# Kernel optimization log

Hardware: AMD Instinct MI355X
Metric: run time of the kernel (lower is better)

## Reference

```python
import jax, jax.numpy as jnp
import numpy as np

N = 20000   # nodes
E = 320000  # edges (before self-loops)
F_IN = 128  # in_feats
H = 4       # heads
C = 64      # hidden (per-head channels; concat=False averages heads)
G = 64      # graphs in batch
EPS = 1e-5  # BatchNorm eps


def _gat(x, src, dst, W, a_src, a_dst, bias):
    # PyG GATConv, concat=False: project, per-edge LeakyReLU attention,
    # segment-softmax over destination nodes, scatter-add, mean over heads.
    h = (x @ W).reshape(N, H, C)                    # [N,H,C]
    es = (h * a_src).sum(-1)                        # [N,H]
    ed = (h * a_dst).sum(-1)                        # [N,H]
    e = jax.nn.leaky_relu(es[src] + ed[dst], 0.2)   # [Etot,H]
    m = jax.ops.segment_max(e, dst, num_segments=N)
    m = jnp.where(jnp.isfinite(m), m, 0.0)          # nodes with no in-edges
    p = jnp.exp(e - m[dst])
    s = jax.ops.segment_sum(p, dst, num_segments=N)
    alpha = p / (s[dst] + 1e-16)                    # PyG softmax epsilon
    out = jax.ops.segment_sum(h[src] * alpha[:, :, None], dst, num_segments=N)
    return out.mean(axis=1) + bias                  # [N,C]


def _bn(x, g, b):
    # BatchNorm1d in training mode: biased batch statistics over nodes
    mu = x.mean(axis=0)
    var = ((x - mu) ** 2).mean(axis=0)
    return (x - mu) * jax.lax.rsqrt(var + EPS) * g + b


def setup_inputs() -> dict:
    key = jax.random.key(0)
    ks = jax.random.split(key, 16)
    x = jax.random.normal(ks[0], (N, F_IN), dtype=jnp.float32)
    edge_index = jax.random.randint(ks[1], (2, E), 0, N, dtype=jnp.int32)
    batch_idx = jnp.sort(jax.random.randint(ks[2], (N,), 0, G, dtype=jnp.int32))
    s1 = 1.0 / np.sqrt(F_IN)
    s2 = 1.0 / np.sqrt(C)
    return {
        "x": x,
        "W1": jax.random.normal(ks[3], (F_IN, H * C), jnp.float32) * s1,
        "a_src1": jax.random.normal(ks[4], (H, C), jnp.float32) * s2,
        "a_dst1": jax.random.normal(ks[5], (H, C), jnp.float32) * s2,
        "b1": jnp.zeros((C,), jnp.float32),
        "Wskip": jax.random.normal(ks[6], (F_IN, C), jnp.float32) * s1,
        "bskip": jnp.zeros((C,), jnp.float32),
        "g1": jnp.ones((C,), jnp.float32),
        "be1": jnp.zeros((C,), jnp.float32),
        "W2": jax.random.normal(ks[7], (C, H * C), jnp.float32) * s2,
        "a_src2": jax.random.normal(ks[8], (H, C), jnp.float32) * s2,
        "a_dst2": jax.random.normal(ks[9], (H, C), jnp.float32) * s2,
        "b2": jnp.zeros((C,), jnp.float32),
        "g2": jnp.ones((C,), jnp.float32),
        "be2": jnp.zeros((C,), jnp.float32),
        "edge_index": edge_index,
        "batch_idx": batch_idx,
    }


def reference(x, W1, a_src1, a_dst1, b1, Wskip, bskip, g1, be1,
              W2, a_src2, a_dst2, b2, g2, be2, edge_index, batch_idx):
    # add self-loops (PyG GATConv default add_self_loops=True)
    loop = jnp.arange(N, dtype=edge_index.dtype)
    src = jnp.concatenate([edge_index[0], loop])
    dst = jnp.concatenate([edge_index[1], loop])

    x0 = x
    h = _gat(x, src, dst, W1, a_src1, a_dst1, b1)
    h = jax.nn.gelu(_bn(h, g1, be1) + x0 @ Wskip + bskip, approximate=False)
    # dropout is identity in eval mode
    h2 = _gat(h, src, dst, W2, a_src2, a_dst2, b2)
    h2 = jax.nn.gelu(_bn(h2, g2, be2) + h, approximate=False)

    # global mean pool over graphs
    sums = jax.ops.segment_sum(h2, batch_idx, num_segments=G)
    cnts = jax.ops.segment_sum(jnp.ones((N,), h2.dtype), batch_idx, num_segments=G)
    return sums / jnp.maximum(cnts, 1.0)[:, None]
```

## Files before the change

kernel.cpp:

```cpp
#include <hip/hip_runtime.h>
#include <math.h>

#define NN   20000
#define EE   320000
#define ETOT 340000
#define FIN  128
#define HH   4
#define CC   64
#define HC   256
#define GG   64
#define BN_EPS 1e-5f
#define S1   384
#define S2   320
#define NBUCK 64
#define MAXDEG 64

typedef _Float16 v8h __attribute__((ext_vector_type(8)));
typedef _Float16 v4h __attribute__((ext_vector_type(4)));
typedef float    v4f __attribute__((ext_vector_type(4)));

__device__ __forceinline__ unsigned short f2bf(float f) {
    unsigned u = __float_as_uint(f);
    unsigned r = (u + 0x7FFF + ((u >> 16) & 1)) >> 16;
    return (unsigned short)r;
}
__device__ __forceinline__ float bf2f(unsigned short u) {
    return __uint_as_float((unsigned)u << 16);
}
__device__ __forceinline__ float gelu_exact(float v) {
    return 0.5f * v * (1.f + erff(v * 0.70710678118654752f));
}

__global__ __launch_bounds__(256) void pre1_kernel(
        const int* __restrict__ bidx, int* __restrict__ gstart,
        const float* __restrict__ W1, const float* __restrict__ Wskip,
        const float* __restrict__ W2,
        const float* __restrict__ as1, const float* __restrict__ ad1,
        const float* __restrict__ as2, const float* __restrict__ ad2,
        _Float16* __restrict__ BT1, _Float16* __restrict__ BT2,
        int* __restrict__ deg, float* __restrict__ sbuck1,
        float* __restrict__ sbuck2, float* __restrict__ outz) {
    int b = blockIdx.x, t = threadIdx.x;
    if (b < 79) {
        int i = b * 256 + t;
        if (i >= NN) return;
        int cur = bidx[i];
        if (i == 0) { for (int g = 0; g <= cur; ++g) gstart[g] = 0; }
        else { int prev = bidx[i - 1]; for (int g = prev + 1; g <= cur; ++g) gstart[g] = i; }
        if (i == NN - 1) { for (int g = cur + 1; g <= GG; ++g) gstart[g] = NN; }
    } else if (b < 271) {
        int i = (b - 79) * 256 + t;
        int col = i >> 7, k = i & 127;
        float v;
        if (col < 256) {
            v = W1[k * 256 + (col & 3) * 64 + (col >> 2)];
        } else if (col < 320) {
            v = Wskip[k * 64 + (col - 256)];
        } else if (col < 328) {
            int kk = col - 320, h = kk & 3;
            const float* av = (kk < 4 ? as1 : ad1) + h * 64;
            const float* wr = W1 + k * 256 + h * 64;
            float s = 0.f;
            #pragma unroll 8
            for (int c = 0; c < 64; ++c) s += wr[c] * av[c];
            v = s;
        } else v = 0.f;
        BT1[i] = (_Float16)v;
    } else if (b < 351) {
        int i = (b - 271) * 256 + t;
        int col = i >> 6, k = i & 63;
        float v;
        if (col < 256) {
            v = W2[k * 256 + (col & 3) * 64 + (col >> 2)];
        } else if (col < 264) {
            int kk = col - 256, h = kk & 3;
            const float* av = (kk < 4 ? as2 : ad2) + h * 64;
            const float* wr = W2 + k * 256 + h * 64;
            float s = 0.f;
            #pragma unroll 8
            for (int c = 0; c < 64; ++c) s += wr[c] * av[c];
            v = s;
        } else v = 0.f;
        BT2[i] = (_Float16)v;
    } else if (b < 367) {
        int i = (b - 351) * 256 + t;
        outz[i] = 0.f;
    } else if (b < 446) {
        int i = (b - 367) * 256 + t;
        if (i < NN) deg[i] = 0;
    } else if (b < 478) {
        int i = (b - 446) * 256 + t;
        sbuck1[i] = 0.f;
    } else {
        int i = (b - 478) * 256 + t;
        sbuck2[i] = 0.f;
    }
}

template<int NCB>
__global__ __launch_bounds__(256) void gemm_mfma(const float* __restrict__ A,
        const _Float16* __restrict__ BT, int M, int K,
        unsigned short* __restrict__ h4b, float* __restrict__ skipO,
        float* __restrict__ esf, float* __restrict__ edf,
        int escol0, int ngemm, int do_fill,
        const int* __restrict__ ei, int* __restrict__ deg,
        int* __restrict__ csr) {
    int b = blockIdx.x;
    int t = threadIdx.x;
    if (do_fill && b >= ngemm) {
        int i = (b - ngemm) * 256 + t;
        if (i >= ETOT) return;
        int s, d;
        if (i < EE) { s = ei[i]; d = ei[EE + i]; } else { s = i - EE; d = i - EE; }
        int p = atomicAdd(&deg[d], 1);
        if (p < MAXDEG) csr[d * MAXDEG + p] = s;
        return;
    }
    const int COLT = 2 * NCB * 16;
    __shared__ _Float16 sA[32][40];
    __shared__ _Float16 sBT[2 * NCB * 16][40];
    int tile = b & 1;
    int col0 = tile * COLT;
    int row0 = (b >> 1) * 32;
    int wave = t >> 6, lane = t & 63;
    int l15 = lane & 15, quad = lane >> 4;
    int rb  = wave & 1;
    int cb0 = (wave >> 1) * NCB;
    v4f acc[NCB] = {};
    for (int k0 = 0; k0 < K; k0 += 32) {
        {
            int r = t >> 3, c4 = t & 7;
            int gr = row0 + r;
            float4 v0 = make_float4(0.f, 0.f, 0.f, 0.f);
            if (gr < M) v0 = *(const float4*)&A[(size_t)gr * K + k0 + c4 * 4];
            v4h hv;
            hv[0] = (_Float16)v0.x; hv[1] = (_Float16)v0.y;
            hv[2] = (_Float16)v0.z; hv[3] = (_Float16)v0.w;
            *(v4h*)&sA[r][c4 * 4] = hv;
        }
        for (int j = t; j < COLT * 4; j += 256) {
            int c = j >> 2, s = j & 3;
            *(v8h*)&sBT[c][s * 8] = *(const v8h*)&BT[(size_t)(col0 + c) * K + k0 + s * 8];
        }
        __syncthreads();
        v8h af = *(const v8h*)&sA[rb * 16 + l15][quad * 8];
        #pragma unroll
        for (int c = 0; c < NCB; ++c) {
            v8h bf = *(const v8h*)&sBT[(cb0 + c) * 16 + l15][quad * 8];
            acc[c] = __builtin_amdgcn_mfma_f32_16x16x32_f16(af, bf, acc[c], 0, 0, 0);
        }
        __syncthreads();
    }
    #pragma unroll
    for (int c = 0; c < NCB; ++c) {
        int gcol = col0 + (cb0 + c) * 16 + l15;
        #pragma unroll
        for (int reg = 0; reg < 4; ++reg) {
            int gr = row0 + rb * 16 + quad * 4 + reg;
            if (gr >= M) continue;
            float v = acc[c][reg];
            if (gcol < 256) {
                h4b[(size_t)gr * HC + gcol] = f2bf(v);
            } else if (skipO != nullptr && gcol < 320) {
                skipO[(size_t)gr * CC + (gcol - 256)] = v;
            } else if (gcol >= escol0 && gcol < escol0 + 8) {
                if (gcol < escol0 + 4) esf[gr * 4 + (gcol - escol0)] = v;
                else                   edf[gr * 4 + (gcol - escol0 - 4)] = v;
            }
        }
    }
}

template<int NCB>
__global__ __launch_bounds__(256) void gemm_mfma_bn(const float* __restrict__ gout,
        const float* __restrict__ skip, const float* __restrict__ sbuck,
        const float* __restrict__ g, const float* __restrict__ be,
        const float* __restrict__ bskip, float* __restrict__ hmid,
        const _Float16* __restrict__ BT, int M, int K,
        unsigned short* __restrict__ h4b,
        float* __restrict__ esf, float* __restrict__ edf, int escol0) {
    const int COLT = 2 * NCB * 16;
    __shared__ _Float16 sA[32][40];
    __shared__ _Float16 sBT[2 * NCB * 16][40];
    __shared__ float tmp[128];
    __shared__ float sscale[64], sshift[64];
    int t = threadIdx.x;
    int b = blockIdx.x;
    if (t < 128) {
        float s = 0.f;
        #pragma unroll 16
        for (int k = 0; k < NBUCK; ++k) s += sbuck[k * 128 + t];
        tmp[t] = s;
    }
    __syncthreads();
    if (t < 64) {
        float mu  = tmp[t] * (1.f / NN);
        float var = tmp[64 + t] * (1.f / NN) - mu * mu;
        float inv = rsqrtf(var + BN_EPS) * g[t];
        sscale[t] = inv;
        sshift[t] = be[t] + bskip[t] - mu * inv;
    }
    __syncthreads();
    int tile = b & 1;
    int col0 = tile * COLT;
    int row0 = (b >> 1) * 32;
    int wave = t >> 6, lane = t & 63;
    int l15 = lane & 15, quad = lane >> 4;
    int rb  = wave & 1;
    int cb0 = (wave >> 1) * NCB;
    v4f acc[NCB] = {};
    for (int k0 = 0; k0 < K; k0 += 32) {
        {
            int r = t >> 3, c4 = t & 7;
            int gr = row0 + r;
            int cb = k0 + c4 * 4;
            float vv[4];
            if (gr < M) {
                float4 q = *(const float4*)&gout[(size_t)gr * CC + cb];
                float4 p = *(const float4*)&skip[(size_t)gr * CC + cb];
                float qa[4] = {q.x, q.y, q.z, q.w};
                float pa[4] = {p.x, p.y, p.z, p.w};
                #pragma unroll
                for (int u = 0; u < 4; ++u)
                    vv[u] = gelu_exact(qa[u] * sscale[cb + u] + sshift[cb + u] + pa[u]);
                if (tile == 0)
                    *(float4*)&hmid[(size_t)gr * CC + cb] =
                        make_float4(vv[0], vv[1], vv[2], vv[3]);
            } else {
                vv[0] = vv[1] = vv[2] = vv[3] = 0.f;
            }
            v4h hv;
            hv[0] = (_Float16)vv[0]; hv[1] = (_Float16)vv[1];
            hv[2] = (_Float16)vv[2]; hv[3] = (_Float16)vv[3];
            *(v4h*)&sA[r][c4 * 4] = hv;
        }
        for (int j = t; j < COLT * 4; j += 256) {
            int c = j >> 2, s = j & 3;
            *(v8h*)&sBT[c][s * 8] = *(const v8h*)&BT[(size_t)(col0 + c) * K + k0 + s * 8];
        }
        __syncthreads();
        v8h af = *(const v8h*)&sA[rb * 16 + l15][quad * 8];
        #pragma unroll
        for (int c = 0; c < NCB; ++c) {
            v8h bf = *(const v8h*)&sBT[(cb0 + c) * 16 + l15][quad * 8];
            acc[c] = __builtin_amdgcn_mfma_f32_16x16x32_f16(af, bf, acc[c], 0, 0, 0);
        }
        __syncthreads();
    }
    #pragma unroll
    for (int c = 0; c < NCB; ++c) {
        int gcol = col0 + (cb0 + c) * 16 + l15;
        #pragma unroll
        for (int reg = 0; reg < 4; ++reg) {
            int gr = row0 + rb * 16 + quad * 4 + reg;
            if (gr >= M) continue;
            float v = acc[c][reg];
            if (gcol < 256) {
                h4b[(size_t)gr * HC + gcol] = f2bf(v);
            } else if (gcol >= escol0 && gcol < escol0 + 8) {
                if (gcol < escol0 + 4) esf[gr * 4 + (gcol - escol0)] = v;
                else                   edf[gr * 4 + (gcol - escol0 - 4)] = v;
            }
        }
    }
}

__device__ __forceinline__ void edge_acc(const float4 esv, const ushort4 hv,
        const float4 edn, float4& acc, float4& ssum) {
    float e0 = esv.x + edn.x; e0 = fmaxf(e0, 0.2f * e0); float w0 = __expf(e0);
    float e1 = esv.y + edn.y; e1 = fmaxf(e1, 0.2f * e1); float w1 = __expf(e1);
    float e2 = esv.z + edn.z; e2 = fmaxf(e2, 0.2f * e2); float w2 = __expf(e2);
    float e3 = esv.w + edn.w; e3 = fmaxf(e3, 0.2f * e3); float w3 = __expf(e3);
    acc.x += w0 * bf2f(hv.x); ssum.x += w0;
    acc.y += w1 * bf2f(hv.y); ssum.y += w1;
    acc.z += w2 * bf2f(hv.z); ssum.z += w2;
    acc.w += w3 * bf2f(hv.w); ssum.w += w3;
}

__global__ __launch_bounds__(256) void aggr_kernel(const unsigned short* __restrict__ h4b,
        const float4* __restrict__ es4, const float4* __restrict__ ed4,
        const int* __restrict__ deg, const int* __restrict__ csr_src,
        const float* __restrict__ bias, float* __restrict__ out,
        float* __restrict__ sbuck) {
    int wave = threadIdx.x >> 6, lane = threadIdx.x & 63;
    int n = blockIdx.x * 4 + wave;
    float4 edn = ed4[n];
    float4 acc = make_float4(0.f, 0.f, 0.f, 0.f);
    float4 ssum = make_float4(0.f, 0.f, 0.f, 0.f);
    int dn = deg[n];
    dn = (dn < MAXDEG) ? dn : MAXDEG;
    int beg = n * MAXDEG, end = beg + dn;
    int j = beg;
    for (; j + 4 <= end; j += 4) {
        int s0 = csr_src[j + 0];
        int s1 = csr_src[j + 1];
        int s2 = csr_src[j + 2];
        int s3 = csr_src[j + 3];
        float4 E0 = es4[s0];
        float4 E1 = es4[s1];
        float4 E2 = es4[s2];
        float4 E3 = es4[s3];
        ushort4 v0 = *(const ushort4*)&h4b[(size_t)s0 * HC + lane * 4];
        ushort4 v1 = *(const ushort4*)&h4b[(size_t)s1 * HC + lane * 4];
        ushort4 v2 = *(const ushort4*)&h4b[(size_t)s2 * HC + lane * 4];
        ushort4 v3 = *(const ushort4*)&h4b[(size_t)s3 * HC + lane * 4];
        edge_acc(E0, v0, edn, acc, ssum);
        edge_acc(E1, v1, edn, acc, ssum);
        edge_acc(E2, v2, edn, acc, ssum);
        edge_acc(E3, v3, edn, acc, ssum);
    }
    for (; j < end; ++j) {
        int s = csr_src[j];
        float4 E = es4[s];
        ushort4 v = *(const ushort4*)&h4b[(size_t)s * HC + lane * 4];
        edge_acc(E, v, edn, acc, ssum);
    }
    float val = 0.25f * (acc.x / (ssum.x + 1e-16f) + acc.y / (ssum.y + 1e-16f) +
                         acc.z / (ssum.z + 1e-16f) + acc.w / (ssum.w + 1e-16f)) + bias[lane];
    out[n * CC + lane] = val;
    __shared__ float ls[4][64], lq[4][64];
    ls[wave][lane] = val;
    lq[wave][lane] = val * val;
    __syncthreads();
    if (wave == 0) {
        float s = ls[0][lane] + ls[1][lane] + ls[2][lane] + ls[3][lane];
        float q = lq[0][lane] + lq[1][lane] + lq[2][lane] + lq[3][lane];
        int bk = (blockIdx.x & (NBUCK - 1)) * 128;
        atomicAdd(&sbuck[bk + lane], s);
        atomicAdd(&sbuck[bk + 64 + lane], q);
    }
}

__global__ __launch_bounds__(256) void bnapply2_kernel(const float* __restrict__ gout,
        const float* __restrict__ sbuck, const float* __restrict__ g,
        const float* __restrict__ be, const float* __restrict__ resid,
        const int* __restrict__ bidx, const int* __restrict__ gstart,
        float* __restrict__ out) {
    __shared__ float tmp[128];
    __shared__ float smu[64], sinv[64];
    __shared__ float ls[4][64];
    __shared__ int gi[4];
    int t = threadIdx.x;
    if (t < 128) {
        float s = 0.f;
        #pragma unroll 16
        for (int k = 0; k < NBUCK; ++k) s += sbuck[k * 128 + t];
        tmp[t] = s;
    }
    __syncthreads();
    if (t < 64) {
        float mu  = tmp[t] * (1.f / NN);
        float var = tmp[64 + t] * (1.f / NN) - mu * mu;
        smu[t] = mu;
        sinv[t] = rsqrtf(var + BN_EPS) * g[t];
    }
    __syncthreads();
    int i = blockIdx.x * 256 + t;
    int ch = i & 63;
    int wave = t >> 6;
    int n = i >> 6;
    float v = (gout[i] - smu[ch]) * sinv[ch] + be[ch] + resid[i];
    v = gelu_exact(v);
    int gg = bidx[n];
    int cnt = gstart[gg + 1] - gstart[gg];
    ls[wave][ch] = v * (1.f / (float)cnt);
    if (ch == 0) gi[wave] = gg;
    __syncthreads();
    if (wave == 0) {
        if (gi[0] == gi[1] && gi[1] == gi[2] && gi[2] == gi[3]) {
            float s = ls[0][ch] + ls[1][ch] + ls[2][ch] + ls[3][ch];
            atomicAdd(&out[gi[0] * CC + ch], s);
        } else {
            #pragma unroll
            for (int w2 = 0; w2 < 4; ++w2)
                atomicAdd(&out[gi[w2] * CC + ch], ls[w2][ch]);
        }
    }
}

extern "C" void kernel_launch(void* const* d_in, const int* in_sizes, int n_in,
                              void* d_out, int out_size, void* d_ws, size_t ws_size,
                              hipStream_t stream) {
    const float* x      = (const float*)d_in[0];
    const float* W1     = (const float*)d_in[1];
    const float* a_src1 = (const float*)d_in[2];
    const float* a_dst1 = (const float*)d_in[3];
    const float* b1     = (const float*)d_in[4];
    const float* Wskip  = (const float*)d_in[5];
    const float* bskip  = (const float*)d_in[6];
    const float* g1     = (const float*)d_in[7];
    const float* be1    = (const float*)d_in[8];
    const float* W2     = (const float*)d_in[9];
    const float* a_src2 = (const float*)d_in[10];
    const float* a_dst2 = (const float*)d_in[11];
    const float* b2     = (const float*)d_in[12];
    const float* g2     = (const float*)d_in[13];
    const float* be2    = (const float*)d_in[14];
    const int*   ei     = (const int*)d_in[15];
    const int*   bidx   = (const int*)d_in[16];
    float* out = (float*)d_out;

    char* w = (char*)d_ws;
    size_t o = 0;
    auto alloc = [&](size_t bytes) -> void* {
        void* p = w + o;
        o = (o + bytes + 255) & ~(size_t)255;
        return p;
    };

    unsigned short* h4b = (unsigned short*)alloc((size_t)NN * HC * 2);
    float4* es4 = (float4*)alloc((size_t)NN * 16);
    float4* ed4 = (float4*)alloc((size_t)NN * 16);
    float* skip = (float*)alloc((size_t)NN * CC * 4);
    float* gout = (float*)alloc((size_t)NN * CC * 4);
    float* hmid = (float*)alloc((size_t)NN * CC * 4);
    _Float16* BT1 = (_Float16*)alloc((size_t)S1 * FIN * 2);
    _Float16* BT2 = (_Float16*)alloc((size_t)S2 * CC * 2);
    int* csr    = (int*)alloc((size_t)NN * MAXDEG * 4);
    int* gstart = (int*)alloc((size_t)(GG + 1) * 4);
    int* deg      = (int*)alloc((size_t)NN * 4);
    float* sbuck1 = (float*)alloc((size_t)NBUCK * 128 * 4);
    float* sbuck2 = (float*)alloc((size_t)NBUCK * 128 * 4);

    int ebk = (ETOT + 255) / 256;
    int nodeblk = NN / 4;

    pre1_kernel<<<510, 256, 0, stream>>>(bidx, gstart,
            W1, Wskip, W2, a_src1, a_dst1, a_src2, a_dst2, BT1, BT2,
            deg, sbuck1, sbuck2, out);

    gemm_mfma<6><<<1250 + ebk, 256, 0, stream>>>(x, BT1, NN, FIN,
            h4b, skip, (float*)es4, (float*)ed4, 320, 1250, 1, ei, deg, csr);
    aggr_kernel<<<nodeblk, 256, 0, stream>>>(h4b, es4, ed4, deg, csr, b1, gout,
            sbuck1);

    gemm_mfma_bn<5><<<1250, 256, 0, stream>>>(gout, skip, sbuck1, g1, be1, bskip,
            hmid, BT2, NN, CC, h4b, (float*)es4, (float*)ed4, 256);
    aggr_kernel<<<nodeblk, 256, 0, stream>>>(h4b, es4, ed4, deg, csr, b2, gout,
            sbuck2);
    bnapply2_kernel<<<NN * CC / 256, 256, 0, stream>>>(
        gout, sbuck2, g2, be2, hmid, bidx, gstart, out);
}
```

Measured before the change: 214.1 us.

## Fuse all stages into one persistent cooperative kernel with grid syncs

Replaces the six separate kernel launches (prep, GEMM1+CSR fill, aggregation, BN+GEMM2, aggregation, BN+pool) with a single cooperative persistent kernel that loops over work units and separates phases with grid.sync(). The aim is to remove per-launch overhead and inter-kernel gaps. In exchange, occupancy is capped by the cooperative grid size and by the register and shared-memory footprint of the merged kernel, and each grid-wide barrier has its own cost. The BN scale/shift is now computed once per block instead of once per GEMM block.

```diff
diff --git a/kernel.cpp b/kernel.cpp
--- a/kernel.cpp
+++ b/kernel.cpp
@@ -1,5 +1,8 @@
 #include <hip/hip_runtime.h>
+#include <hip/hip_cooperative_groups.h>
 #include <math.h>
+
+namespace cg = cooperative_groups;
 
 #define NN   20000
 #define EE   320000
@@ -14,6 +17,7 @@
 #define S2   320
 #define NBUCK 64
 #define MAXDEG 64
+#define EBK  1329
 
 typedef _Float16 v8h __attribute__((ext_vector_type(8)));
 typedef _Float16 v4h __attribute__((ext_vector_type(4)));
@@ -31,97 +35,34 @@
     return 0.5f * v * (1.f + erff(v * 0.70710678118654752f));
 }
 
-__global__ __launch_bounds__(256) void pre1_kernel(
-        const int* __restrict__ bidx, int* __restrict__ gstart,
-        const float* __restrict__ W1, const float* __restrict__ Wskip,
-        const float* __restrict__ W2,
-        const float* __restrict__ as1, const float* __restrict__ ad1,
-        const float* __restrict__ as2, const float* __restrict__ ad2,
-        _Float16* __restrict__ BT1, _Float16* __restrict__ BT2,
-        int* __restrict__ deg, float* __restrict__ sbuck1,
-        float* __restrict__ sbuck2, float* __restrict__ outz) {
-    int b = blockIdx.x, t = threadIdx.x;
-    if (b < 79) {
-        int i = b * 256 + t;
-        if (i >= NN) return;
-        int cur = bidx[i];
-        if (i == 0) { for (int g = 0; g <= cur; ++g) gstart[g] = 0; }
-        else { int prev = bidx[i - 1]; for (int g = prev + 1; g <= cur; ++g) gstart[g] = i; }
-        if (i == NN - 1) { for (int g = cur + 1; g <= GG; ++g) gstart[g] = NN; }
-    } else if (b < 271) {
-        int i = (b - 79) * 256 + t;
-        int col = i >> 7, k = i & 127;
-        float v;
-        if (col < 256) {
-            v = W1[k * 256 + (col & 3) * 64 + (col >> 2)];
-        } else if (col < 320) {
-            v = Wskip[k * 64 + (col - 256)];
-        } else if (col < 328) {
-            int kk = col - 320, h = kk & 3;
-            const float* av = (kk < 4 ? as1 : ad1) + h * 64;
-            const float* wr = W1 + k * 256 + h * 64;
-            float s = 0.f;
-            #pragma unroll 8
-            for (int c = 0; c < 64; ++c) s += wr[c] * av[c];
-            v = s;
-        } else v = 0.f;
-        BT1[i] = (_Float16)v;
-    } else if (b < 351) {
-        int i = (b - 271) * 256 + t;
-        int col = i >> 6, k = i & 63;
-        float v;
-        if (col < 256) {
-            v = W2[k * 256 + (col & 3) * 64 + (col >> 2)];
-        } else if (col < 264) {
-            int kk = col - 256, h = kk & 3;
-            const float* av = (kk < 4 ? as2 : ad2) + h * 64;
-            const float* wr = W2 + k * 256 + h * 64;
-            float s = 0.f;
-            #pragma unroll 8
-            for (int c = 0; c < 64; ++c) s += wr[c] * av[c];
-            v = s;
-        } else v = 0.f;
-        BT2[i] = (_Float16)v;
-    } else if (b < 367) {
-        int i = (b - 351) * 256 + t;
-        outz[i] = 0.f;
-    } else if (b < 446) {
-        int i = (b - 367) * 256 + t;
-        if (i < NN) deg[i] = 0;
-    } else if (b < 478) {
-        int i = (b - 446) * 256 + t;
-        sbuck1[i] = 0.f;
-    } else {
-        int i = (b - 478) * 256 + t;
-        sbuck2[i] = 0.f;
-    }
-}
-
-template<int NCB>
-__global__ __launch_bounds__(256) void gemm_mfma(const float* __restrict__ A,
+struct MegaParams {
+    const float* x;
+    const float* W1; const float* as1; const float* ad1; const float* b1;
+    const float* Wskip; const float* bskip; const float* g1; const float* be1;
+    const float* W2; const float* as2; const float* ad2; const float* b2;
+    const float* g2; const float* be2;
+    const int* ei; const int* bidx;
+    float* out;
+    unsigned short* h4b;
+    float4* es4; float4* ed4;
+    float* skip; float* gout; float* hmid;
+    _Float16* BT1; _Float16* BT2;
+    int* csr; int* gstart; int* deg;
+    float* sbuck1; float* sbuck2;
+};
+
+template<int NCB, bool BN>
+__device__ __forceinline__ void gemm_unit(int u,
+        const float* __restrict__ A, const float* __restrict__ skipIn,
+        float* __restrict__ hmid, const float* sscale, const float* sshift,
         const _Float16* __restrict__ BT, int M, int K,
         unsigned short* __restrict__ h4b, float* __restrict__ skipO,
-        float* __restrict__ esf, float* __restrict__ edf,
-        int escol0, int ngemm, int do_fill,
-        const int* __restrict__ ei, int* __restrict__ deg,
-        int* __restrict__ csr) {
-    int b = blockIdx.x;
-    int t = threadIdx.x;
-    if (do_fill && b >= ngemm) {
-        int i = (b - ngemm) * 256 + t;
-        if (i >= ETOT) return;
-        int s, d;
-        if (i < EE) { s = ei[i]; d = ei[EE + i]; } else { s = i - EE; d = i - EE; }
-        int p = atomicAdd(&deg[d], 1);
-        if (p < MAXDEG) csr[d * MAXDEG + p] = s;
-        return;
-    }
+        float* __restrict__ esf, float* __restrict__ edf, int escol0,
+        _Float16 (*sA)[40], _Float16 (*sBT)[40], int t) {
     const int COLT = 2 * NCB * 16;
-    __shared__ _Float16 sA[32][40];
-    __shared__ _Float16 sBT[2 * NCB * 16][40];
-    int tile = b & 1;
+    int tile = u & 1;
     int col0 = tile * COLT;
-    int row0 = (b >> 1) * 32;
+    int row0 = (u >> 1) * 32;
     int wave = t >> 6, lane = t & 63;
     int l15 = lane & 15, quad = lane >> 4;
     int rb  = wave & 1;
@@ -131,11 +72,28 @@
         {
             int r = t >> 3, c4 = t & 7;
             int gr = row0 + r;
-            float4 v0 = make_float4(0.f, 0.f, 0.f, 0.f);
-            if (gr < M) v0 = *(const float4*)&A[(size_t)gr * K + k0 + c4 * 4];
+            int cb = k0 + c4 * 4;
+            float vv[4] = {0.f, 0.f, 0.f, 0.f};
+            if (gr < M) {
+                if constexpr (BN) {
+                    float4 q = *(const float4*)&A[(size_t)gr * K + cb];
+                    float4 p = *(const float4*)&skipIn[(size_t)gr * K + cb];
+                    float qa[4] = {q.x, q.y, q.z, q.w};
+                    float pa[4] = {p.x, p.y, p.z, p.w};
+                    #pragma unroll
+                    for (int uu = 0; uu < 4; ++uu)
+                        vv[uu] = gelu_exact(qa[uu] * sscale[cb + uu] + sshift[cb + uu] + pa[uu]);
+                    if (tile == 0)
+                        *(float4*)&hmid[(size_t)gr * K + cb] =
+                            make_float4(vv[0], vv[1], vv[2], vv[3]);
+                } else {
+                    float4 v0 = *(const float4*)&A[(size_t)gr * K + cb];
+                    vv[0] = v0.x; vv[1] = v0.y; vv[2] = v0.z; vv[3] = v0.w;
+                }
+            }
             v4h hv;
-            hv[0] = (_Float16)v0.x; hv[1] = (_Float16)v0.y;
-            hv[2] = (_Float16)v0.z; hv[3] = (_Float16)v0.w;
+            hv[0] = (_Float16)vv[0]; hv[1] = (_Float16)vv[1];
+            hv[2] = (_Float16)vv[2]; hv[3] = (_Float16)vv[3];
             *(v4h*)&sA[r][c4 * 4] = hv;
         }
         for (int j = t; j < COLT * 4; j += 256) {
@@ -171,100 +129,6 @@
     }
 }
 
-template<int NCB>
-__global__ __launch_bounds__(256) void gemm_mfma_bn(const float* __restrict__ gout,
-        const float* __restrict__ skip, const float* __restrict__ sbuck,
-        const float* __restrict__ g, const float* __restrict__ be,
-        const float* __restrict__ bskip, float* __restrict__ hmid,
-        const _Float16* __restrict__ BT, int M, int K,
-        unsigned short* __restrict__ h4b,
-        float* __restrict__ esf, float* __restrict__ edf, int escol0) {
-    const int COLT = 2 * NCB * 16;
-    __shared__ _Float16 sA[32][40];
-    __shared__ _Float16 sBT[2 * NCB * 16][40];
-    __shared__ float tmp[128];
-    __shared__ float sscale[64], sshift[64];
-    int t = threadIdx.x;
-    int b = blockIdx.x;
-    if (t < 128) {
-        float s = 0.f;
-        #pragma unroll 16
-        for (int k = 0; k < NBUCK; ++k) s += sbuck[k * 128 + t];
-        tmp[t] = s;
-    }
-    __syncthreads();
-    if (t < 64) {
-        float mu  = tmp[t] * (1.f / NN);
-        float var = tmp[64 + t] * (1.f / NN) - mu * mu;
-        float inv = rsqrtf(var + BN_EPS) * g[t];
-        sscale[t] = inv;
-        sshift[t] = be[t] + bskip[t] - mu * inv;
-    }
-    __syncthreads();
-    int tile = b & 1;
-    int col0 = tile * COLT;
-    int row0 = (b >> 1) * 32;
-    int wave = t >> 6, lane = t & 63;
-    int l15 = lane & 15, quad = lane >> 4;
-    int rb  = wave & 1;
-    int cb0 = (wave >> 1) * NCB;
-    v4f acc[NCB] = {};
-    for (int k0 = 0; k0 < K; k0 += 32) {
-        {
-            int r = t >> 3, c4 = t & 7;
-            int gr = row0 + r;
-            int cb = k0 + c4 * 4;
-            float vv[4];
-            if (gr < M) {
-                float4 q = *(const float4*)&gout[(size_t)gr * CC + cb];
-                float4 p = *(const float4*)&skip[(size_t)gr * CC + cb];
-                float qa[4] = {q.x, q.y, q.z, q.w};
-                float pa[4] = {p.x, p.y, p.z, p.w};
-                #pragma unroll
-                for (int u = 0; u < 4; ++u)
-                    vv[u] = gelu_exact(qa[u] * sscale[cb + u] + sshift[cb + u] + pa[u]);
-                if (tile == 0)
-                    *(float4*)&hmid[(size_t)gr * CC + cb] =
-                        make_float4(vv[0], vv[1], vv[2], vv[3]);
-            } else {
-                vv[0] = vv[1] = vv[2] = vv[3] = 0.f;
-            }
-            v4h hv;
-            hv[0] = (_Float16)vv[0]; hv[1] = (_Float16)vv[1];
-            hv[2] = (_Float16)vv[2]; hv[3] = (_Float16)vv[3];
-            *(v4h*)&sA[r][c4 * 4] = hv;
-        }
-        for (int j = t; j < COLT * 4; j += 256) {
-            int c = j >> 2, s = j & 3;
-            *(v8h*)&sBT[c][s * 8] = *(const v8h*)&BT[(size_t)(col0 + c) * K + k0 + s * 8];
-        }
-        __syncthreads();
-        v8h af = *(const v8h*)&sA[rb * 16 + l15][quad * 8];
-        #pragma unroll
-        for (int c = 0; c < NCB; ++c) {
-            v8h bf = *(const v8h*)&sBT[(cb0 + c) * 16 + l15][quad * 8];
-            acc[c] = __builtin_amdgcn_mfma_f32_16x16x32_f16(af, bf, acc[c], 0, 0, 0);
-        }
-        __syncthreads();
-    }
-    #pragma unroll
-    for (int c = 0; c < NCB; ++c) {
-        int gcol = col0 + (cb0 + c) * 16 + l15;
-        #pragma unroll
-        for (int reg = 0; reg < 4; ++reg) {
-            int gr = row0 + rb * 16 + quad * 4 + reg;
-            if (gr >= M) continue;
-            float v = acc[c][reg];
-            if (gcol < 256) {
-                h4b[(size_t)gr * HC + gcol] = f2bf(v);
-            } else if (gcol >= escol0 && gcol < escol0 + 8) {
-                if (gcol < escol0 + 4) esf[gr * 4 + (gcol - escol0)] = v;
-                else                   edf[gr * 4 + (gcol - escol0 - 4)] = v;
-            }
-        }
-    }
-}
-
 __device__ __forceinline__ void edge_acc(const float4 esv, const ushort4 hv,
         const float4 edn, float4& acc, float4& ssum) {
     float e0 = esv.x + edn.x; e0 = fmaxf(e0, 0.2f * e0); float w0 = __expf(e0);
@@ -277,13 +141,13 @@
     acc.w += w3 * bf2f(hv.w); ssum.w += w3;
 }
 
-__global__ __launch_bounds__(256) void aggr_kernel(const unsigned short* __restrict__ h4b,
+__device__ __forceinline__ void aggr_unit(int u, const unsigned short* __restrict__ h4b,
         const float4* __restrict__ es4, const float4* __restrict__ ed4,
         const int* __restrict__ deg, const int* __restrict__ csr_src,
         const float* __restrict__ bias, float* __restrict__ out,
-        float* __restrict__ sbuck) {
-    int wave = threadIdx.x >> 6, lane = threadIdx.x & 63;
-    int n = blockIdx.x * 4 + wave;
+        float* __restrict__ sbuck, float* sls, int t) {
+    int wave = t >> 6, lane = t & 63;
+    int n = u * 4 + wave;
     float4 edn = ed4[n];
     float4 acc = make_float4(0.f, 0.f, 0.f, 0.f);
     float4 ssum = make_float4(0.f, 0.f, 0.f, 0.f);
@@ -318,62 +182,181 @@
     float val = 0.25f * (acc.x / (ssum.x + 1e-16f) + acc.y / (ssum.y + 1e-16f) +
                          acc.z / (ssum.z + 1e-16f) + acc.w / (ssum.w + 1e-16f)) + bias[lane];
     out[n * CC + lane] = val;
-    __shared__ float ls[4][64], lq[4][64];
+    float (*ls)[64] = (float (*)[64])sls;
+    float (*lq)[64] = (float (*)[64])(sls + 256);
     ls[wave][lane] = val;
     lq[wave][lane] = val * val;
     __syncthreads();
     if (wave == 0) {
         float s = ls[0][lane] + ls[1][lane] + ls[2][lane] + ls[3][lane];
         float q = lq[0][lane] + lq[1][lane] + lq[2][lane] + lq[3][lane];
-        int bk = (blockIdx.x & (NBUCK - 1)) * 128;
+        int bk = (u & (NBUCK - 1)) * 128;
         atomicAdd(&sbuck[bk + lane], s);
         atomicAdd(&sbuck[bk + 64 + lane], q);
     }
-}
-
-__global__ __launch_bounds__(256) void bnapply2_kernel(const float* __restrict__ gout,
-        const float* __restrict__ sbuck, const float* __restrict__ g,
-        const float* __restrict__ be, const float* __restrict__ resid,
-        const int* __restrict__ bidx, const int* __restrict__ gstart,
-        float* __restrict__ out) {
-    __shared__ float tmp[128];
-    __shared__ float smu[64], sinv[64];
-    __shared__ float ls[4][64];
+    __syncthreads();
+}
+
+__global__ __launch_bounds__(256) void mega(MegaParams P) {
+    cg::grid_group grid = cg::this_grid();
+    __shared__ __align__(16) unsigned char smem[17920];
+    __shared__ float sS[64], sH[64];
     __shared__ int gi[4];
     int t = threadIdx.x;
-    if (t < 128) {
-        float s = 0.f;
-        #pragma unroll 16
-        for (int k = 0; k < NBUCK; ++k) s += sbuck[k * 128 + t];
-        tmp[t] = s;
-    }
-    __syncthreads();
-    if (t < 64) {
-        float mu  = tmp[t] * (1.f / NN);
-        float var = tmp[64 + t] * (1.f / NN) - mu * mu;
-        smu[t] = mu;
-        sinv[t] = rsqrtf(var + BN_EPS) * g[t];
-    }
-    __syncthreads();
-    int i = blockIdx.x * 256 + t;
-    int ch = i & 63;
-    int wave = t >> 6;
-    int n = i >> 6;
-    float v = (gout[i] - smu[ch]) * sinv[ch] + be[ch] + resid[i];
-    v = gelu_exact(v);
-    int gg = bidx[n];
-    int cnt = gstart[gg + 1] - gstart[gg];
-    ls[wave][ch] = v * (1.f / (float)cnt);
-    if (ch == 0) gi[wave] = gg;
-    __syncthreads();
-    if (wave == 0) {
-        if (gi[0] == gi[1] && gi[1] == gi[2] && gi[2] == gi[3]) {
-            float s = ls[0][ch] + ls[1][ch] + ls[2][ch] + ls[3][ch];
-            atomicAdd(&out[gi[0] * CC + ch], s);
+    int nG = gridDim.x;
+
+    for (int u = blockIdx.x; u < 510; u += nG) {
+        if (u < 79) {
+            int i = u * 256 + t;
+            if (i < NN) {
+                int cur = P.bidx[i];
+                if (i == 0) { for (int g = 0; g <= cur; ++g) P.gstart[g] = 0; }
+                else { int prev = P.bidx[i - 1]; for (int g = prev + 1; g <= cur; ++g) P.gstart[g] = i; }
+                if (i == NN - 1) { for (int g = cur + 1; g <= GG; ++g) P.gstart[g] = NN; }
+            }
+        } else if (u < 271) {
+            int i = (u - 79) * 256 + t;
+            int col = i >> 7, k = i & 127;
+            float v;
+            if (col < 256) {
+                v = P.W1[k * 256 + (col & 3) * 64 + (col >> 2)];
+            } else if (col < 320) {
+                v = P.Wskip[k * 64 + (col - 256)];
+            } else if (col < 328) {
+                int kk = col - 320, h = kk & 3;
+                const float* av = (kk < 4 ? P.as1 : P.ad1) + h * 64;
+                const float* wr = P.W1 + k * 256 + h * 64;
+                float sdot = 0.f;
+                #pragma unroll 8
+                for (int c = 0; c < 64; ++c) sdot += wr[c] * av[c];
+                v = sdot;
+            } else v = 0.f;
+            P.BT1[i] = (_Float16)v;
+        } else if (u < 351) {
+            int i = (u - 271) * 256 + t;
+            int col = i >> 6, k = i & 63;
+            float v;
+            if (col < 256) {
+                v = P.W2[k * 256 + (col & 3) * 64 + (col >> 2)];
+            } else if (col < 264) {
+                int kk = col - 256, h = kk & 3;
+                const float* av = (kk < 4 ? P.as2 : P.ad2) + h * 64;
+                const float* wr = P.W2 + k * 256 + h * 64;
+                float sdot = 0.f;
+                #pragma unroll 8
+                for (int c = 0; c < 64; ++c) sdot += wr[c] * av[c];
+                v = sdot;
+            } else v = 0.f;
+            P.BT2[i] = (_Float16)v;
+        } else if (u < 367) {
+            int i = (u - 351) * 256 + t;
+            P.out[i] = 0.f;
+        } else if (u < 446) {
+            int i = (u - 367) * 256 + t;
+            if (i < NN) P.deg[i] = 0;
+        } else if (u < 478) {
+            int i = (u - 446) * 256 + t;
+            P.sbuck1[i] = 0.f;
         } else {
-            #pragma unroll
-            for (int w2 = 0; w2 < 4; ++w2)
-                atomicAdd(&out[gi[w2] * CC + ch], ls[w2][ch]);
+            int i = (u - 478) * 256 + t;
+            P.sbuck2[i] = 0.f;
+        }
+    }
+    grid.sync();
+
+    _Float16 (*sA)[40]  = (_Float16 (*)[40])smem;
+    _Float16 (*sBT)[40] = (_Float16 (*)[40])(smem + 32 * 40 * 2);
+    float* sls = (float*)smem;
+
+    for (int u = blockIdx.x; u < 1250 + EBK; u += nG) {
+        if (u < 1250) {
+            gemm_unit<6, false>(u, P.x, nullptr, nullptr, nullptr, nullptr,
+                P.BT1, NN, FIN, P.h4b, P.skip, (float*)P.es4, (float*)P.ed4, 320,
+                sA, sBT, t);
+        } else {
+            int i = (u - 1250) * 256 + t;
+            if (i < ETOT) {
+                int s, d;
+                if (i < EE) { s = P.ei[i]; d = P.ei[EE + i]; } else { s = i - EE; d = i - EE; }
+                int pp = atomicAdd(&P.deg[d], 1);
+                if (pp < MAXDEG) P.csr[d * MAXDEG + pp] = s;
+            }
+        }
+    }
+    grid.sync();
+
+    for (int u = blockIdx.x; u < 5000; u += nG)
+        aggr_unit(u, P.h4b, P.es4, P.ed4, P.deg, P.csr, P.b1, P.gout, P.sbuck1, sls, t);
+    grid.sync();
+
+    {
+        float* tmp = (float*)smem;
+        if (t < 128) {
+            float s = 0.f;
+            #pragma unroll 16
+            for (int k = 0; k < NBUCK; ++k) s += P.sbuck1[k * 128 + t];
+            tmp[t] = s;
+        }
+        __syncthreads();
+        if (t < 64) {
+            float mu  = tmp[t] * (1.f / NN);
+            float var = tmp[64 + t] * (1.f / NN) - mu * mu;
+            float inv = rsqrtf(var + BN_EPS) * P.g1[t];
+            sS[t] = inv;
+            sH[t] = P.be1[t] + P.bskip[t] - mu * inv;
+        }
+        __syncthreads();
+    }
+    for (int u = blockIdx.x; u < 1250; u += nG)
+        gemm_unit<5, true>(u, P.gout, P.skip, P.hmid, sS, sH,
+            P.BT2, NN, CC, P.h4b, nullptr, (float*)P.es4, (float*)P.ed4, 256,
+            sA, sBT, t);
+    grid.sync();
+
+    for (int u = blockIdx.x; u < 5000; u += nG)
+        aggr_unit(u, P.h4b, P.es4, P.ed4, P.deg, P.csr, P.b2, P.gout, P.sbuck2, sls, t);
+    grid.sync();
+
+    {
+        float* tmp = (float*)smem;
+        if (t < 128) {
+            float s = 0.f;
+            #pragma unroll 16
+            for (int k = 0; k < NBUCK; ++k) s += P.sbuck2[k * 128 + t];
+            tmp[t] = s;
+        }
+        __syncthreads();
+        if (t < 64) {
+            float mu  = tmp[t] * (1.f / NN);
+            float var = tmp[64 + t] * (1.f / NN) - mu * mu;
+            sS[t] = mu;
+            sH[t] = rsqrtf(var + BN_EPS) * P.g2[t];
+        }
+        __syncthreads();
+        float (*ls)[64] = (float (*)[64])smem;
+        for (int u = blockIdx.x; u < 5000; u += nG) {
+            int i = u * 256 + t;
+            int ch = i & 63;
+            int wave = t >> 6;
+            int n = i >> 6;
+            float v = (P.gout[i] - sS[ch]) * sH[ch] + P.be2[ch] + P.hmid[i];
+            v = gelu_exact(v);
+            int gg = P.bidx[n];
+            int cnt = P.gstart[gg + 1] - P.gstart[gg];
+            ls[wave][ch] = v * (1.f / (float)cnt);
+            if (ch == 0) gi[wave] = gg;
+            __syncthreads();
+            if (wave == 0) {
+                if (gi[0] == gi[1] && gi[1] == gi[2] && gi[2] == gi[3]) {
+                    float s4 = ls[0][ch] + ls[1][ch] + ls[2][ch] + ls[3][ch];
+                    atomicAdd(&P.out[gi[0] * CC + ch], s4);
+                } else {
+                    #pragma unroll
+                    for (int w2 = 0; w2 < 4; ++w2)
+                        atomicAdd(&P.out[gi[w2] * CC + ch], ls[w2][ch]);
+                }
+            }
+            __syncthreads();
         }
     }
 }
@@ -381,24 +364,25 @@
 extern "C" void kernel_launch(void* const* d_in, const int* in_sizes, int n_in,
                               void* d_out, int out_size, void* d_ws, size_t ws_size,
                               hipStream_t stream) {
-    const float* x      = (const float*)d_in[0];
-    const float* W1     = (const float*)d_in[1];
-    const float* a_src1 = (const float*)d_in[2];
-    const float* a_dst1 = (const float*)d_in[3];
-    const float* b1     = (const float*)d_in[4];
-    const float* Wskip  = (const float*)d_in[5];
-    const float* bskip  = (const float*)d_in[6];
-    const float* g1     = (const float*)d_in[7];
-    const float* be1    = (const float*)d_in[8];
-    const float* W2     = (const float*)d_in[9];
-    const float* a_src2 = (const float*)d_in[10];
-    const float* a_dst2 = (const float*)d_in[11];
-    const float* b2     = (const float*)d_in[12];
-    const float* g2     = (const float*)d_in[13];
-    const float* be2    = (const float*)d_in[14];
-    const int*   ei     = (const int*)d_in[15];
-    const int*   bidx   = (const int*)d_in[16];
-    float* out = (float*)d_out;
+    MegaParams P;
+    P.x      = (const float*)d_in[0];
+    P.W1     = (const float*)d_in[1];
+    P.as1    = (const float*)d_in[2];
+    P.ad1    = (const float*)d_in[3];
+    P.b1     = (const float*)d_in[4];
+    P.Wskip  = (const float*)d_in[5];
+    P.bskip  = (const float*)d_in[6];
+    P.g1     = (const float*)d_in[7];
+    P.be1    = (const float*)d_in[8];
+    P.W2     = (const float*)d_in[9];
+    P.as2    = (const float*)d_in[10];
+    P.ad2    = (const float*)d_in[11];
+    P.b2     = (const float*)d_in[12];
+    P.g2     = (const float*)d_in[13];
+    P.be2    = (const float*)d_in[14];
+    P.ei     = (const int*)d_in[15];
+    P.bidx   = (const int*)d_in[16];
+    P.out    = (float*)d_out;
 
     char* w = (char*)d_ws;
     size_t o = 0;
@@ -407,37 +391,32 @@
         o = (o + bytes + 255) & ~(size_t)255;
         return p;
     };
-
-    unsigned short* h4b = (unsigned short*)alloc((size_t)NN * HC * 2);
-    float4* es4 = (float4*)alloc((size_t)NN * 16);
-    float4* ed4 = (float4*)alloc((size_t)NN * 16);
-    float* skip = (float*)alloc((size_t)NN * CC * 4);
-    float* gout = (float*)alloc((size_t)NN * CC * 4);
-    float* hmid = (float*)alloc((size_t)NN * CC * 4);
-    _Float16* BT1 = (_Float16*)alloc((size_t)S1 * FIN * 2);
-    _Float16* BT2 = (_Float16*)alloc((size_t)S2 * CC * 2);
-    int* csr    = (int*)alloc((size_t)NN * MAXDEG * 4);
-    int* gstart = (int*)alloc((size_t)(GG + 1) * 4);
-    int* deg      = (int*)alloc((size_t)NN * 4);
-    float* sbuck1 = (float*)alloc((size_t)NBUCK * 128 * 4);
-    float* sbuck2 = (float*)alloc((size_t)NBUCK * 128 * 4);
-
-    int ebk = (ETOT + 255) / 256;
-    int nodeblk = NN / 4;
-
-    pre1_kernel<<<510, 256, 0, stream>>>(bidx, gstart,
-            W1, Wskip, W2, a_src1, a_dst1, a_src2, a_dst2, BT1, BT2,
-            deg, sbuck1, sbuck2, out);
-
-    gemm_mfma<6><<<1250 + ebk, 256, 0, stream>>>(x, BT1, NN, FIN,
-            h4b, skip, (float*)es4, (float*)ed4, 320, 1250, 1, ei, deg, csr);
-    aggr_kernel<<<nodeblk, 256, 0, stream>>>(h4b, es4, ed4, deg, csr, b1, gout,
-            sbuck1);
-
-    gemm_mfma_bn<5><<<1250, 256, 0, stream>>>(gout, skip, sbuck1, g1, be1, bskip,
-            hmid, BT2, NN, CC, h4b, (float*)es4, (float*)ed4, 256);
-    aggr_kernel<<<nodeblk, 256, 0, stream>>>(h4b, es4, ed4, deg, csr, b2, gout,
-            sbuck2);
-    bnapply2_kernel<<<NN * CC / 256, 256, 0, stream>>>(
-        gout, sbuck2, g2, be2, hmid, bidx, gstart, out);
-}
+    P.h4b  = (unsigned short*)alloc((size_t)NN * HC * 2);
+    P.es4  = (float4*)alloc((size_t)NN * 16);
+    P.ed4  = (float4*)alloc((size_t)NN * 16);
+    P.skip = (float*)alloc((size_t)NN * CC * 4);
+    P.gout = (float*)alloc((size_t)NN * CC * 4);
+    P.hmid = (float*)alloc((size_t)NN * CC * 4);
+    P.BT1  = (_Float16*)alloc((size_t)S1 * FIN * 2);
+    P.BT2  = (_Float16*)alloc((size_t)S2 * CC * 2);
+    P.csr  = (int*)alloc((size_t)NN * MAXDEG * 4);
+    P.gstart = (int*)alloc((size_t)(GG + 1) * 4);
+    P.deg    = (int*)alloc((size_t)NN * 4);
+    P.sbuck1 = (float*)alloc((size_t)NBUCK * 128 * 4);
+    P.sbuck2 = (float*)alloc((size_t)NBUCK * 128 * 4);
+
+    static int gblocks = 0;
+    if (gblocks == 0) {
+        int nb = 0, dev = 0, cus = 0;
+        hipGetDevice(&dev);
+        hipDeviceGetAttribute(&cus, hipDeviceAttributeMultiprocessorCount, dev);
+        hipOccupancyMaxActiveBlocksPerMultiprocessor(&nb, mega, 256, 0);
+        if (cus <= 0) cus = 256;
+        if (nb <= 0) nb = 1;
+        long long g = (long long)nb * cus;
+        if (g > 2048) g = 2048;
+        gblocks = (int)g;
+    }
+    void* args[] = { (void*)&P };
+    hipLaunchCooperativeKernel(mega, dim3(gblocks), dim3(256), args, 0, stream);
+}
```

Result: slower. 610.9 us (+185.3%).

## Store projected features head-major so each lane aggregates one head's channels

Applied to the files above, without the earlier changes.

The packed weight matrices now keep W1/W2 columns in natural head-major order instead of an interleaved channel-major order. The aggregation kernel changes to match: each lane handles four channels of a single head, so it loads one scalar attention logit per edge and computes one exp instead of four. The per-node results are then reduced across heads with cross-lane shuffles, and only 16 lanes write float4 outputs. This cuts redundant exp and softmax-sum work per edge, at the cost of shuffle reductions and fewer active lanes in the epilogue.

```diff
diff --git a/kernel.cpp b/kernel.cpp
--- a/kernel.cpp
+++ b/kernel.cpp
@@ -53,7 +53,7 @@
         int col = i >> 7, k = i & 127;
         float v;
         if (col < 256) {
-            v = W1[k * 256 + (col & 3) * 64 + (col >> 2)];
+            v = W1[k * 256 + col];
         } else if (col < 320) {
             v = Wskip[k * 64 + (col - 256)];
         } else if (col < 328) {
@@ -71,7 +71,7 @@
         int col = i >> 6, k = i & 63;
         float v;
         if (col < 256) {
-            v = W2[k * 256 + (col & 3) * 64 + (col >> 2)];
+            v = W2[k * 256 + col];
         } else if (col < 264) {
             int kk = col - 256, h = kk & 3;
             const float* av = (kk < 4 ? as2 : ad2) + h * 64;
@@ -265,28 +265,17 @@
     }
 }
 
-__device__ __forceinline__ void edge_acc(const float4 esv, const ushort4 hv,
-        const float4 edn, float4& acc, float4& ssum) {
-    float e0 = esv.x + edn.x; e0 = fmaxf(e0, 0.2f * e0); float w0 = __expf(e0);
-    float e1 = esv.y + edn.y; e1 = fmaxf(e1, 0.2f * e1); float w1 = __expf(e1);
-    float e2 = esv.z + edn.z; e2 = fmaxf(e2, 0.2f * e2); float w2 = __expf(e2);
-    float e3 = esv.w + edn.w; e3 = fmaxf(e3, 0.2f * e3); float w3 = __expf(e3);
-    acc.x += w0 * bf2f(hv.x); ssum.x += w0;
-    acc.y += w1 * bf2f(hv.y); ssum.y += w1;
-    acc.z += w2 * bf2f(hv.z); ssum.z += w2;
-    acc.w += w3 * bf2f(hv.w); ssum.w += w3;
-}
-
 __global__ __launch_bounds__(256) void aggr_kernel(const unsigned short* __restrict__ h4b,
-        const float4* __restrict__ es4, const float4* __restrict__ ed4,
+        const float* __restrict__ esf, const float* __restrict__ edf,
         const int* __restrict__ deg, const int* __restrict__ csr_src,
         const float* __restrict__ bias, float* __restrict__ out,
         float* __restrict__ sbuck) {
     int wave = threadIdx.x >> 6, lane = threadIdx.x & 63;
+    int head = lane >> 4;
     int n = blockIdx.x * 4 + wave;
-    float4 edn = ed4[n];
+    float edn = edf[n * 4 + head];
     float4 acc = make_float4(0.f, 0.f, 0.f, 0.f);
-    float4 ssum = make_float4(0.f, 0.f, 0.f, 0.f);
+    float ssum = 0.f;
     int dn = deg[n];
     dn = (dn < MAXDEG) ? dn : MAXDEG;
     int beg = n * MAXDEG, end = beg + dn;
@@ -296,31 +285,54 @@
         int s1 = csr_src[j + 1];
         int s2 = csr_src[j + 2];
         int s3 = csr_src[j + 3];
-        float4 E0 = es4[s0];
-        float4 E1 = es4[s1];
-        float4 E2 = es4[s2];
-        float4 E3 = es4[s3];
+        float E0 = esf[s0 * 4 + head];
+        float E1 = esf[s1 * 4 + head];
+        float E2 = esf[s2 * 4 + head];
+        float E3 = esf[s3 * 4 + head];
         ushort4 v0 = *(const ushort4*)&h4b[(size_t)s0 * HC + lane * 4];
         ushort4 v1 = *(const ushort4*)&h4b[(size_t)s1 * HC + lane * 4];
         ushort4 v2 = *(const ushort4*)&h4b[(size_t)s2 * HC + lane * 4];
         ushort4 v3 = *(const ushort4*)&h4b[(size_t)s3 * HC + lane * 4];
-        edge_acc(E0, v0, edn, acc, ssum);
-        edge_acc(E1, v1, edn, acc, ssum);
-        edge_acc(E2, v2, edn, acc, ssum);
-        edge_acc(E3, v3, edn, acc, ssum);
+        float e0 = E0 + edn; e0 = fmaxf(e0, 0.2f * e0); float w0 = __expf(e0);
+        float e1 = E1 + edn; e1 = fmaxf(e1, 0.2f * e1); float w1 = __expf(e1);
+        float e2 = E2 + edn; e2 = fmaxf(e2, 0.2f * e2); float w2 = __expf(e2);
+        float e3 = E3 + edn; e3 = fmaxf(e3, 0.2f * e3); float w3 = __expf(e3);
+        acc.x += w0 * bf2f(v0.x); acc.y += w0 * bf2f(v0.y);
+        acc.z += w0 * bf2f(v0.z); acc.w += w0 * bf2f(v0.w); ssum += w0;
+        acc.x += w1 * bf2f(v1.x); acc.y += w1 * bf2f(v1.y);
+        acc.z += w1 * bf2f(v1.z); acc.w += w1 * bf2f(v1.w); ssum += w1;
+        acc.x += w2 * bf2f(v2.x); acc.y += w2 * bf2f(v2.y);
+        acc.z += w2 * bf2f(v2.z); acc.w += w2 * bf2f(v2.w); ssum += w2;
+        acc.x += w3 * bf2f(v3.x); acc.y += w3 * bf2f(v3.y);
+        acc.z += w3 * bf2f(v3.z); acc.w += w3 * bf2f(v3.w); ssum += w3;
     }
     for (; j < end; ++j) {
         int s = csr_src[j];
-        float4 E = es4[s];
+        float E = esf[s * 4 + head];
         ushort4 v = *(const ushort4*)&h4b[(size_t)s * HC + lane * 4];
-        edge_acc(E, v, edn, acc, ssum);
-    }
-    float val = 0.25f * (acc.x / (ssum.x + 1e-16f) + acc.y / (ssum.y + 1e-16f) +
-                         acc.z / (ssum.z + 1e-16f) + acc.w / (ssum.w + 1e-16f)) + bias[lane];
-    out[n * CC + lane] = val;
+        float e = E + edn; e = fmaxf(e, 0.2f * e); float w = __expf(e);
+        acc.x += w * bf2f(v.x); acc.y += w * bf2f(v.y);
+        acc.z += w * bf2f(v.z); acc.w += w * bf2f(v.w); ssum += w;
+    }
+    float inv = 1.f / (ssum + 1e-16f);
+    float4 r;
+    r.x = acc.x * inv; r.y = acc.y * inv; r.z = acc.z * inv; r.w = acc.w * inv;
+    r.x += __shfl_xor(r.x, 16); r.y += __shfl_xor(r.y, 16);
+    r.z += __shfl_xor(r.z, 16); r.w += __shfl_xor(r.w, 16);
+    r.x += __shfl_xor(r.x, 32); r.y += __shfl_xor(r.y, 32);
+    r.z += __shfl_xor(r.z, 32); r.w += __shfl_xor(r.w, 32);
     __shared__ float ls[4][64], lq[4][64];
-    ls[wave][lane] = val;
-    lq[wave][lane] = val * val;
+    if (lane < 16) {
+        float4 b4 = *(const float4*)&bias[lane * 4];
+        float4 o;
+        o.x = 0.25f * r.x + b4.x; o.y = 0.25f * r.y + b4.y;
+        o.z = 0.25f * r.z + b4.z; o.w = 0.25f * r.w + b4.w;
+        *(float4*)&out[n * CC + lane * 4] = o;
+        *(float4*)&ls[wave][lane * 4] = o;
+        float4 q;
+        q.x = o.x * o.x; q.y = o.y * o.y; q.z = o.z * o.z; q.w = o.w * o.w;
+        *(float4*)&lq[wave][lane * 4] = q;
+    }
     __syncthreads();
     if (wave == 0) {
         float s = ls[0][lane] + ls[1][lane] + ls[2][lane] + ls[3][lane];
@@ -409,8 +421,8 @@
     };
 
     unsigned short* h4b = (unsigned short*)alloc((size_t)NN * HC * 2);
-    float4* es4 = (float4*)alloc((size_t)NN * 16);
-    float4* ed4 = (float4*)alloc((size_t)NN * 16);
+    float* esf = (float*)alloc((size_t)NN * 16);
+    float* edf = (float*)alloc((size_t)NN * 16);
     float* skip = (float*)alloc((size_t)NN * CC * 4);
     float* gout = (float*)alloc((size_t)NN * CC * 4);
     float* hmid = (float*)alloc((size_t)NN * CC * 4);
@@ -430,13 +442,13 @@
             deg, sbuck1, sbuck2, out);
 
     gemm_mfma<6><<<1250 + ebk, 256, 0, stream>>>(x, BT1, NN, FIN,
-            h4b, skip, (float*)es4, (float*)ed4, 320, 1250, 1, ei, deg, csr);
-    aggr_kernel<<<nodeblk, 256, 0, stream>>>(h4b, es4, ed4, deg, csr, b1, gout,
+            h4b, skip, esf, edf, 320, 1250, 1, ei, deg, csr);
+    aggr_kernel<<<nodeblk, 256, 0, stream>>>(h4b, esf, edf, deg, csr, b1, gout,
             sbuck1);
 
     gemm_mfma_bn<5><<<1250, 256, 0, stream>>>(gout, skip, sbuck1, g1, be1, bskip,
-            hmid, BT2, NN, CC, h4b, (float*)es4, (float*)ed4, 256);
-    aggr_kernel<<<nodeblk, 256, 0, stream>>>(h4b, es4, ed4, deg, csr, b2, gout,
+            hmid, BT2, NN, CC, h4b, esf, edf, 256);
+    aggr_kernel<<<nodeblk, 256, 0, stream>>>(h4b, esf, edf, deg, csr, b2, gout,
             sbuck2);
     bnapply2_kernel<<<NN * CC / 256, 256, 0, stream>>>(
         gout, sbuck2, g2, be2, hmid, bidx, gstart, out);
```

Result: faster. 200.2 us (-6.5%).
